# Kernel tuning notes

Hardware: AMD Instinct MI355X
Metric: run time of the kernel (lower is better)

The kernel has to match this reference:

```python
import jax, jax.numpy as jnp
import numpy as np

H, DH = 8, 64           # heads, dim_head
SCALE = DH ** -0.5


def setup_inputs() -> dict:
    key = jax.random.key(0)
    ks = jax.random.split(key, 8)
    b, f, n, dim = 16, 8, 256, 512
    inner = H * DH
    w = lambda k, s: jax.random.normal(k, s, jnp.float32) * 0.02
    return {
        "x": jax.random.normal(ks[0], (b, f * n, dim), jnp.float32),
        "external": jax.random.normal(ks[1], (b, 1, dim), jnp.float32),
        "Wq": w(ks[2], (dim, inner)), "bq": jnp.zeros((inner,), jnp.float32),
        "Wk": w(ks[3], (dim, inner)), "bk": jnp.zeros((inner,), jnp.float32),
        "Wv": w(ks[4], (dim, inner)), "bv": jnp.zeros((inner,), jnp.float32),
        "Wo": w(ks[5], (inner, dim)), "bo": jnp.zeros((dim,), jnp.float32),
        "f": f,
    }


def reference(x, external, Wq, bq, Wk, bk, Wv, bv, Wo, bo, f):
    b, N, dim = x.shape          # N = f * n
    n = N // f
    xa = jnp.concatenate([external, x], axis=1)          # (b, N+1, dim)

    def proj(W, bias):
        t = xa @ W + bias                                # (b, N+1, H*DH)
        # 'b n (h d) -> (b h) n d'
        return t.reshape(b, N + 1, H, DH).transpose(0, 2, 1, 3).reshape(b * H, N + 1, DH)

    q = proj(Wq, bq) * SCALE
    k = proj(Wk, bk)
    v = proj(Wv, bv)

    def split_local(t):
        ext = jnp.repeat(t[:, :1], f, axis=0)            # (b*H*f, 1, DH)  'b n d -> (b r) n d'
        loc = t[:, 1:].reshape(b * H * f, n, DH)         # 'b (f n) d -> (b f) n d'
        return jnp.concatenate([ext, loc], axis=1)       # (b*H*f, n+1, DH)

    q_, k_, v_ = split_local(q), split_local(k), split_local(v)

    att = jax.nn.softmax(jnp.einsum('bid,bjd->bij', q_, k_), axis=-1)
    out = jnp.einsum('bij,bjd->bid', att, v_)            # (b*H*f, n+1, DH)

    # external token output: '(b h r) d -> b r (h d)' then take r == 1
    ext_out = out[:, 0].reshape(b, H, f, DH).transpose(0, 2, 1, 3).reshape(b, f, H * DH)
    ext_out = ext_out[:, 1:2]                            # (b, 1, H*DH)

    # local outputs: '(b f) n d -> b (f n) d' then '(b h) n d -> b n (h d)'
    main = out[:, 1:].reshape(b, H, N, DH).transpose(0, 2, 1, 3).reshape(b, N, H * DH)

    return main @ Wo + bo, ext_out @ Wo + bo
```

## Files before the change

### kernel.cpp

```cpp
#include <hip/hip_runtime.h>
#include <stdint.h>

#define ATT_SCALE 0.125f

typedef __attribute__((ext_vector_type(8))) short bhalf8;
typedef __attribute__((ext_vector_type(4))) float floatx4;
typedef __attribute__((ext_vector_type(16))) float floatx16;
typedef __attribute__((ext_vector_type(8))) unsigned short ush8;

__device__ __forceinline__ unsigned short f2bf(float f) {
  union { float f; unsigned int u; } v; v.f = f;
  unsigned int r = v.u + 0x7fffu + ((v.u >> 16) & 1u);
  return (unsigned short)(r >> 16);
}
__device__ __forceinline__ float bf2f(unsigned short u) {
  union { unsigned int u; float f; } v; v.u = ((unsigned int)u) << 16;
  return v.f;
}
__device__ __forceinline__ unsigned int pk2(float a, float b) {
  unsigned int r;
  asm("v_cvt_pk_bf16_f32 %0, %1, %2" : "=v"(r) : "v"(a), "v"(b));
  return r;
}
__device__ __forceinline__ void glds16(const void* g, void* l) {
  __builtin_amdgcn_global_load_lds(
      (__attribute__((address_space(1))) void*)g,
      (__attribute__((address_space(3))) void*)l, 16, 0, 0);
}

__global__ __launch_bounds__(256) void k_conv_w(
    const float* __restrict__ Wq, const float* __restrict__ Wk,
    const float* __restrict__ Wv, const float* __restrict__ Wo,
    const float* __restrict__ bq, const float* __restrict__ bk, const float* __restrict__ bv,
    unsigned short* __restrict__ Wqkvt, unsigned short* __restrict__ Wot,
    float* __restrict__ biasqkv) {
  int idx = blockIdx.x * 256 + threadIdx.x;
  {
    int nn = idx >> 9, k = idx & 511;
    const float* W = (nn < 512) ? Wq : ((nn < 1024) ? Wk : Wv);
    int n = nn & 511;
    Wqkvt[idx] = f2bf(W[k * 512 + n]);
  }
  if (idx < 512 * 512) {
    int n = idx >> 9, k = idx & 511;
    Wot[idx] = f2bf(Wo[k * 512 + n]);
  }
  if (idx < 1536) {
    biasqkv[idx] = (idx < 512) ? bq[idx] : ((idx < 1024) ? bk[idx - 512] : bv[idx - 1024]);
  }
}

__global__ __launch_bounds__(256) void k_ext_qkv(
    const float* __restrict__ ext,
    const float* __restrict__ Wq, const float* __restrict__ Wk, const float* __restrict__ Wv,
    const float* __restrict__ bq, const float* __restrict__ bk, const float* __restrict__ bv,
    float* __restrict__ EQKV) {
  int b = blockIdx.x / 6, c = blockIdx.x % 6;
  int nn = c * 256 + threadIdx.x;
  __shared__ float xs[512];
  xs[threadIdx.x] = ext[b * 512 + threadIdx.x];
  xs[256 + threadIdx.x] = ext[b * 512 + 256 + threadIdx.x];
  __syncthreads();
  const float* W; const float* bias; float scale = 1.f; int n;
  if (nn < 512)      { W = Wq; bias = bq; n = nn;        scale = ATT_SCALE; }
  else if (nn < 1024){ W = Wk; bias = bk; n = nn - 512; }
  else               { W = Wv; bias = bv; n = nn - 1024; }
  float acc = 0.f;
  #pragma unroll 8
  for (int k = 0; k < 512; ++k) acc += xs[k] * W[k * 512 + n];
  EQKV[b * 1536 + nn] = (acc + bias[n]) * scale;
}

__global__ __launch_bounds__(256, 2) void k_gemm_qkv(
    const float* __restrict__ X, const unsigned short* __restrict__ B,
    const float* __restrict__ bias, unsigned short* __restrict__ C) {
  __shared__ __align__(16) float Af[8192];
  __shared__ __align__(16) unsigned short Bs[8192];
  int tid = threadIdx.x, lane = tid & 63, wv = tid >> 6;
  int lo = lane & 15, hi = lane >> 4;
  int waveM = wv >> 1, waveN = wv & 1;

  int nwg = gridDim.x;
  int wg = (blockIdx.x & 7) * (nwg >> 3) + (blockIdx.x >> 3);
  int bm = wg / 12, bn = wg % 12;

  const float* Xb = X + (size_t)bm * 128 * 512;
  const unsigned short* Bb = B + (size_t)bn * 128 * 512;

  floatx4 acc[4][4];
  #pragma unroll
  for (int m = 0; m < 4; ++m)
    #pragma unroll
    for (int n = 0; n < 4; ++n) acc[m][n] = floatx4{0.f, 0.f, 0.f, 0.f};

  for (int kt = 0; kt < 8; ++kt) {
    __syncthreads();
    #pragma unroll
    for (int i = 0; i < 8; ++i) {
      int chunk = i * 256 + tid;
      int row = chunk >> 4, slot = chunk & 15;
      glds16(Xb + (size_t)row * 512 + kt * 64 + ((slot ^ (row & 15)) << 2),
             Af + (size_t)(i * 256 + wv * 64) * 4);
    }
    #pragma unroll
    for (int i = 0; i < 4; ++i) {
      int chunk = i * 256 + tid;
      int row = chunk >> 3, slot = chunk & 7;
      glds16(Bb + (size_t)row * 512 + kt * 64 + ((slot ^ (row & 7)) << 3),
             Bs + (size_t)(i * 256 + wv * 64) * 8);
    }
    __syncthreads();

    bhalf8 af[4][2], bf4[4][2];
    #pragma unroll
    for (int m = 0; m < 4; ++m) {
      int row = waveM * 64 + m * 16 + lo;
      #pragma unroll
      for (int ks = 0; ks < 2; ++ks) {
        int j0 = (ks * 4 + hi) * 2;
        float4 fa = *(const float4*)(Af + (size_t)row * 64 + ((j0 ^ (row & 15)) << 2));
        float4 fb = *(const float4*)(Af + (size_t)row * 64 + (((j0 + 1) ^ (row & 15)) << 2));
        unsigned int* w = (unsigned int*)&af[m][ks];
        w[0] = pk2(fa.x, fa.y); w[1] = pk2(fa.z, fa.w);
        w[2] = pk2(fb.x, fb.y); w[3] = pk2(fb.z, fb.w);
      }
    }
    #pragma unroll
    for (int n = 0; n < 4; ++n) {
      int row = waveN * 64 + n * 16 + lo;
      #pragma unroll
      for (int ks = 0; ks < 2; ++ks)
        bf4[n][ks] = *(const bhalf8*)(Bs + (size_t)row * 64 + (((ks * 4 + hi) ^ (row & 7)) << 3));
    }
    #pragma unroll
    for (int m = 0; m < 4; ++m)
      #pragma unroll
      for (int n = 0; n < 4; ++n) {
        acc[m][n] = __builtin_amdgcn_mfma_f32_16x16x32_bf16(af[m][0], bf4[n][0], acc[m][n], 0, 0, 0);
        acc[m][n] = __builtin_amdgcn_mfma_f32_16x16x32_bf16(af[m][1], bf4[n][1], acc[m][n], 0, 0, 0);
      }
  }

  #pragma unroll
  for (int m = 0; m < 4; ++m) {
    int row0 = bm * 128 + waveM * 64 + m * 16 + hi * 4;
    #pragma unroll
    for (int n = 0; n < 4; ++n) {
      int col = bn * 128 + waveN * 64 + n * 16 + lo;
      float bb = bias[col];
      #pragma unroll
      for (int r = 0; r < 4; ++r) {
        float v = acc[m][n][r] + bb;
        if (col < 512) v *= ATT_SCALE;
        C[(size_t)(row0 + r) * 1536 + col] = f2bf(v);
      }
    }
  }
}

__global__ __launch_bounds__(256, 2) void k_gemm_out(
    const unsigned short* __restrict__ A, const unsigned short* __restrict__ B,
    const float* __restrict__ bias, float* __restrict__ C) {
  __shared__ __align__(16) unsigned short S[16384];
  int tid = threadIdx.x, lane = tid & 63, wv = tid >> 6;
  int lo = lane & 15, hi = lane >> 4;
  int waveM = wv >> 1, waveN = wv & 1;

  int nwg = gridDim.x;
  int wg = (blockIdx.x & 7) * (nwg >> 3) + (blockIdx.x >> 3);
  int bm = wg / 4, bn = wg % 4;

  const unsigned short* Ab = A + (size_t)bm * 128 * 512;
  const unsigned short* Bb = B + (size_t)bn * 128 * 512;
  unsigned short* lA = S;
  unsigned short* lB = S + 8192;

  floatx4 acc[4][4];
  #pragma unroll
  for (int m = 0; m < 4; ++m)
    #pragma unroll
    for (int n = 0; n < 4; ++n) acc[m][n] = floatx4{0.f, 0.f, 0.f, 0.f};

  for (int kt = 0; kt < 8; ++kt) {
    __syncthreads();
    #pragma unroll
    for (int i = 0; i < 4; ++i) {
      int chunk = i * 256 + tid;
      int row = chunk >> 3, slot = chunk & 7;
      glds16(Ab + (size_t)row * 512 + kt * 64 + ((slot ^ (row & 7)) << 3),
             lA + (size_t)(i * 256 + wv * 64) * 8);
    }
    #pragma unroll
    for (int i = 0; i < 4; ++i) {
      int chunk = i * 256 + tid;
      int row = chunk >> 3, slot = chunk & 7;
      glds16(Bb + (size_t)row * 512 + kt * 64 + ((slot ^ (row & 7)) << 3),
             lB + (size_t)(i * 256 + wv * 64) * 8);
    }
    __syncthreads();

    bhalf8 af[4][2], bf4[4][2];
    #pragma unroll
    for (int m = 0; m < 4; ++m) {
      int row = waveM * 64 + m * 16 + lo;
      #pragma unroll
      for (int ks = 0; ks < 2; ++ks)
        af[m][ks] = *(const bhalf8*)(lA + (size_t)row * 64 + (((ks * 4 + hi) ^ (row & 7)) << 3));
    }
    #pragma unroll
    for (int n = 0; n < 4; ++n) {
      int row = waveN * 64 + n * 16 + lo;
      #pragma unroll
      for (int ks = 0; ks < 2; ++ks)
        bf4[n][ks] = *(const bhalf8*)(lB + (size_t)row * 64 + (((ks * 4 + hi) ^ (row & 7)) << 3));
    }
    #pragma unroll
    for (int m = 0; m < 4; ++m)
      #pragma unroll
      for (int n = 0; n < 4; ++n) {
        acc[m][n] = __builtin_amdgcn_mfma_f32_16x16x32_bf16(af[m][0], bf4[n][0], acc[m][n], 0, 0, 0);
        acc[m][n] = __builtin_amdgcn_mfma_f32_16x16x32_bf16(af[m][1], bf4[n][1], acc[m][n], 0, 0, 0);
      }
  }

  #pragma unroll
  for (int m = 0; m < 4; ++m) {
    int row0 = bm * 128 + waveM * 64 + m * 16 + hi * 4;
    #pragma unroll
    for (int n = 0; n < 4; ++n) {
      int col = bn * 128 + waveN * 64 + n * 16 + lo;
      float bb = bias[col];
      #pragma unroll
      for (int r = 0; r < 4; ++r)
        C[(size_t)(row0 + r) * 512 + col] = acc[m][n][r] + bb;
    }
  }
}

#define VTC 296
__global__ __launch_bounds__(512, 4) void k_attn(
    const unsigned short* __restrict__ QKV,
    const float* __restrict__ EQKV,
    unsigned short* __restrict__ mainb) {
  __shared__ __align__(16) unsigned short Ks[256 * 64];
  __shared__ __align__(16) unsigned short Vt[64 * VTC];
  __shared__ float kx[64], vx[64];
  int g = blockIdx.x;
  int b = g >> 6, h = (g >> 3) & 7, j = g & 7;
  int tid = threadIdx.x, lane = tid & 63, wv = tid >> 6;
  int ql = lane & 31, hb = lane >> 5;
  const size_t rowbase = (size_t)b * 2048 + (size_t)j * 256;
  const unsigned short* Kg = QKV + rowbase * 1536 + 512 + h * 64;
  const unsigned short* Vg = QKV + rowbase * 1536 + 1024 + h * 64;

  int qbase = wv * 32;
  const unsigned short* qp = QKV + (rowbase + qbase + ql) * 1536 + h * 64 + hb * 8;
  bhalf8 qf[4];
  #pragma unroll
  for (int c = 0; c < 4; ++c) qf[c] = *(const bhalf8*)(qp + c * 16);

  {
    int keybase = wv * 32;
    #pragma unroll
    for (int i = 0; i < 4; ++i) {
      int key = keybase + i * 8 + (lane >> 3);
      int slot = lane & 7;
      const unsigned short* src =
          Kg + (size_t)key * 1536 + (((slot * 16) ^ ((key & 7) << 4)) >> 1);
      glds16(src, &Ks[(size_t)(keybase + i * 8) * 64]);
    }
  }
  for (int c = tid; c < 2048; c += 512) {
    int key = c & 255, d0 = (c >> 8) * 8;
    ush8 vv = *(const ush8*)(Vg + (size_t)key * 1536 + d0);
    #pragma unroll
    for (int u = 0; u < 8; ++u) Vt[(d0 + u) * VTC + key] = vv[u];
  }
  if (tid < 64) {
    kx[tid] = EQKV[b * 1536 + 512 + h * 64 + tid];
    vx[tid] = EQKV[b * 1536 + 1024 + h * 64 + tid];
  }
  __syncthreads();

  float part = 0.f;
  #pragma unroll
  for (int c = 0; c < 4; ++c)
    #pragma unroll
    for (int u = 0; u < 8; ++u)
      part += bf2f((unsigned short)qf[c][u]) * kx[c * 16 + hb * 8 + u];
  float m = part + __shfl_xor(part, 32, 64);
  float lsum = 1.f;
  floatx16 o0, o1;
  #pragma unroll
  for (int i = 0; i < 8; ++i) {
    int d0 = ((2 * i) & 3) + 8 * (i >> 1) + 4 * hb;
    o0[2 * i] = vx[d0];       o0[2 * i + 1] = vx[d0 + 1];
    o1[2 * i] = vx[32 + d0];  o1[2 * i + 1] = vx[32 + d0 + 1];
  }

  #pragma unroll
  for (int t = 0; t < 8; ++t) {
    floatx16 s;
    #pragma unroll
    for (int i = 0; i < 16; ++i) s[i] = 0.f;
    int key = t * 32 + ql;
    __builtin_amdgcn_s_setprio(1);
    #pragma unroll
    for (int c = 0; c < 4; ++c) {
      bhalf8 kf = *(const bhalf8*)((const char*)Ks + key * 128 +
                                   ((c * 32 + hb * 16) ^ ((key & 7) << 4)));
      s = __builtin_amdgcn_mfma_f32_32x32x16_bf16(kf, qf[c], s, 0, 0, 0);
    }
    __builtin_amdgcn_s_setprio(0);
    float mt = s[0];
    #pragma unroll
    for (int r = 1; r < 16; ++r) mt = fmaxf(mt, s[r]);
    mt = fmaxf(mt, __shfl_xor(mt, 32, 64));
    if (!__all(mt - m <= 8.f)) {
      float mnew = fmaxf(m, mt);
      float corr = __expf(m - mnew);
      lsum *= corr;
      #pragma unroll
      for (int r = 0; r < 16; ++r) { o0[r] *= corr; o1[r] *= corr; }
      m = mnew;
    }
    float p[16]; float ts = 0.f;
    #pragma unroll
    for (int r = 0; r < 16; ++r) { p[r] = __expf(s[r] - m); ts += p[r]; }
    lsum += ts;
    unsigned int pk[8], qk[8];
    #pragma unroll
    for (int i = 0; i < 8; ++i) pk[i] = pk2(p[2 * i], p[2 * i + 1]);
    #pragma unroll
    for (int i = 0; i < 8; ++i) qk[i] = __shfl_xor(pk[i], 32, 64);
    bhalf8 f0, f1;
    unsigned int* f0u = (unsigned int*)&f0;
    unsigned int* f1u = (unsigned int*)&f1;
    if (hb == 0) {
      f0u[0] = pk[0]; f0u[1] = pk[1]; f0u[2] = qk[0]; f0u[3] = qk[1];
      f1u[0] = pk[4]; f1u[1] = pk[5]; f1u[2] = qk[4]; f1u[3] = qk[5];
    } else {
      f0u[0] = qk[2]; f0u[1] = qk[3]; f0u[2] = pk[2]; f0u[3] = pk[3];
      f1u[0] = qk[6]; f1u[1] = qk[7]; f1u[2] = pk[6]; f1u[3] = pk[7];
    }
    {
      const char* vb0 = (const char*)Vt + ((0 * 32 + ql) * VTC + t * 32 + hb * 8) * 2;
      bhalf8 v0 = *(const bhalf8*)vb0;
      bhalf8 v1 = *(const bhalf8*)(vb0 + 32);
      const char* vb1 = (const char*)Vt + ((1 * 32 + ql) * VTC + t * 32 + hb * 8) * 2;
      bhalf8 w0 = *(const bhalf8*)vb1;
      bhalf8 w1 = *(const bhalf8*)(vb1 + 32);
      __builtin_amdgcn_s_setprio(1);
      o0 = __builtin_amdgcn_mfma_f32_32x32x16_bf16(v0, f0, o0, 0, 0, 0);
      o0 = __builtin_amdgcn_mfma_f32_32x32x16_bf16(v1, f1, o0, 0, 0, 0);
      o1 = __builtin_amdgcn_mfma_f32_32x32x16_bf16(w0, f0, o1, 0, 0, 0);
      o1 = __builtin_amdgcn_mfma_f32_32x32x16_bf16(w1, f1, o1, 0, 0, 0);
      __builtin_amdgcn_s_setprio(0);
    }
  }

  lsum += __shfl_xor(lsum, 32, 64);
  float rinv = 1.f / lsum;
  __syncthreads();
  char* ob = (char*)(Ks + wv * 2048);
  #pragma unroll
  for (int dt = 0; dt < 2; ++dt) {
    #pragma unroll
    for (int i = 0; i < 8; ++i) {
      int d0 = dt * 32 + ((2 * i) & 3) + 8 * (i >> 1) + 4 * hb;
      float a = (dt ? o1[2 * i] : o0[2 * i]) * rinv;
      float c = (dt ? o1[2 * i + 1] : o0[2 * i + 1]) * rinv;
      *(unsigned int*)(ob + ql * 128 + ((d0 * 2) ^ ((ql & 7) << 4))) = pk2(a, c);
    }
  }
  #pragma unroll
  for (int i = 0; i < 4; ++i) {
    int chunk = i * 64 + lane;
    int q = chunk >> 3, slot = chunk & 7;
    bhalf8 vv = *(const bhalf8*)(ob + q * 128 + ((slot * 16) ^ ((q & 7) << 4)));
    *(bhalf8*)(mainb + (rowbase + qbase + q) * 512 + h * 64 + slot * 8) = vv;
  }
}

__global__ __launch_bounds__(256) void k_ext_attn(
    const unsigned short* __restrict__ QKV, const float* __restrict__ EQKV,
    float* __restrict__ extpre) {
  int b = blockIdx.x >> 3, h = blockIdx.x & 7;
  int tid = threadIdx.x, lane = tid & 63, wv = tid >> 6;
  __shared__ float qs[64];
  __shared__ float ps[257];
  __shared__ float red[8];
  __shared__ float acc4[4][64];
  if (tid < 64) qs[tid] = EQKV[b * 1536 + h * 64 + tid];
  __syncthreads();
  const size_t base = (size_t)b * 2048 + 256;
  float sc[2] = {-1e30f, -1e30f};
  #pragma unroll
  for (int it = 0; it < 2; ++it) {
    int key = tid + it * 256;
    if (key < 257) {
      float s = 0.f;
      if (key == 0) {
        const float* kr = EQKV + b * 1536 + 512 + h * 64;
        #pragma unroll 8
        for (int d = 0; d < 64; ++d) s += qs[d] * kr[d];
      } else {
        const unsigned short* kr = QKV + (base + key - 1) * 1536 + 512 + h * 64;
        #pragma unroll
        for (int c = 0; c < 8; ++c) {
          ush8 kv = *(const ush8*)(kr + c * 8);
          #pragma unroll
          for (int u = 0; u < 8; ++u) s += qs[c * 8 + u] * bf2f(kv[u]);
        }
      }
      sc[it] = s;
    }
  }
  float lmax = fmaxf(sc[0], sc[1]);
  for (int d = 1; d < 64; d <<= 1) lmax = fmaxf(lmax, __shfl_xor(lmax, d, 64));
  if (lane == 0) red[wv] = lmax;
  __syncthreads();
  float M = fmaxf(fmaxf(red[0], red[1]), fmaxf(red[2], red[3]));
  float lsum = 0.f;
  #pragma unroll
  for (int it = 0; it < 2; ++it) {
    int key = tid + it * 256;
    if (key < 257) { float p = __expf(sc[it] - M); ps[key] = p; lsum += p; }
  }
  for (int d = 1; d < 64; d <<= 1) lsum += __shfl_xor(lsum, d, 64);
  if (lane == 0) red[4 + wv] = lsum;
  __syncthreads();
  float S = red[4] + red[5] + red[6] + red[7];
  int d = tid & 63, part = tid >> 6;
  float acc = 0.f;
  for (int key = part; key < 257; key += 4) {
    float vv = (key == 0) ? EQKV[b * 1536 + 1024 + h * 64 + d]
                          : bf2f(QKV[(base + key - 1) * 1536 + 1024 + h * 64 + d]);
    acc += ps[key] * vv;
  }
  acc4[part][d] = acc;
  __syncthreads();
  if (tid < 64) {
    float r = (acc4[0][tid] + acc4[1][tid] + acc4[2][tid] + acc4[3][tid]) / S;
    extpre[b * 512 + h * 64 + tid] = r;
  }
}

__global__ __launch_bounds__(256) void k_ext_out(
    const float* __restrict__ extpre, const float* __restrict__ Wo,
    const float* __restrict__ bo, float* __restrict__ out) {
  int b = blockIdx.x, half = blockIdx.y;
  int n = half * 256 + threadIdx.x;
  __shared__ float xs[512];
  xs[threadIdx.x] = extpre[b * 512 + threadIdx.x];
  xs[256 + threadIdx.x] = extpre[b * 512 + 256 + threadIdx.x];
  __syncthreads();
  float acc = bo[n];
  #pragma unroll 8
  for (int k = 0; k < 512; ++k) acc += xs[k] * Wo[k * 512 + n];
  out[16777216 + b * 512 + n] = acc;
}

extern "C" void kernel_launch(void* const* d_in, const int* in_sizes, int n_in,
                              void* d_out, int out_size, void* d_ws, size_t ws_size,
                              hipStream_t stream) {
  (void)in_sizes; (void)n_in; (void)out_size; (void)ws_size;
  const float* x   = (const float*)d_in[0];
  const float* ext = (const float*)d_in[1];
  const float* Wq  = (const float*)d_in[2];
  const float* bq  = (const float*)d_in[3];
  const float* Wk  = (const float*)d_in[4];
  const float* bk  = (const float*)d_in[5];
  const float* Wv  = (const float*)d_in[6];
  const float* bv  = (const float*)d_in[7];
  const float* Wo  = (const float*)d_in[8];
  const float* bo  = (const float*)d_in[9];
  float* out = (float*)d_out;

  char* ws = (char*)d_ws;
  size_t off = 0;
  auto take = [&](size_t bytes) { char* p = ws + off; off += (bytes + 255) & ~(size_t)255; return p; };
  unsigned short* Wqkvt  = (unsigned short*)take((size_t)1536 * 512 * 2);
  unsigned short* Wot    = (unsigned short*)take((size_t)512 * 512 * 2);
  float*          biasqkv= (float*)take(1536 * 4);
  float*          EQKV   = (float*)take(16 * 1536 * 4);
  unsigned short* QKVb   = (unsigned short*)take((size_t)32768 * 1536 * 2);
  unsigned short* mainb  = (unsigned short*)take((size_t)32768 * 512 * 2);
  float*          extpre = (float*)take(16 * 512 * 4);

  k_conv_w<<<3072, 256, 0, stream>>>(Wq, Wk, Wv, Wo, bq, bk, bv, Wqkvt, Wot, biasqkv);
  k_ext_qkv<<<96, 256, 0, stream>>>(ext, Wq, Wk, Wv, bq, bk, bv, EQKV);
  k_gemm_qkv<<<3072, 256, 0, stream>>>(x, Wqkvt, biasqkv, QKVb);
  k_attn<<<1024, 512, 0, stream>>>(QKVb, EQKV, mainb);
  k_ext_attn<<<128, 256, 0, stream>>>(QKVb, EQKV, extpre);
  k_gemm_out<<<1024, 256, 0, stream>>>(mainb, Wot, bo, out);
  k_ext_out<<<dim3(16, 2), 256, 0, stream>>>(extpre, Wo, bo, out);
}
```

Baseline: 224.6 us.

## Pre-convert X to bf16 and merge small ext kernels into main launches

```diff
diff --git a/kernel.cpp b/kernel.cpp
--- a/kernel.cpp
+++ b/kernel.cpp
@@ -28,54 +28,57 @@
       (__attribute__((address_space(3))) void*)l, 16, 0, 0);
 }
 
-__global__ __launch_bounds__(256) void k_conv_w(
+__global__ __launch_bounds__(256) void k_prep(
+    const float* __restrict__ x, const float* __restrict__ ext,
     const float* __restrict__ Wq, const float* __restrict__ Wk,
     const float* __restrict__ Wv, const float* __restrict__ Wo,
     const float* __restrict__ bq, const float* __restrict__ bk, const float* __restrict__ bv,
-    unsigned short* __restrict__ Wqkvt, unsigned short* __restrict__ Wot,
-    float* __restrict__ biasqkv) {
-  int idx = blockIdx.x * 256 + threadIdx.x;
-  {
-    int nn = idx >> 9, k = idx & 511;
-    const float* W = (nn < 512) ? Wq : ((nn < 1024) ? Wk : Wv);
-    int n = nn & 511;
-    Wqkvt[idx] = f2bf(W[k * 512 + n]);
-  }
-  if (idx < 512 * 512) {
-    int n = idx >> 9, k = idx & 511;
-    Wot[idx] = f2bf(Wo[k * 512 + n]);
-  }
-  if (idx < 1536) {
-    biasqkv[idx] = (idx < 512) ? bq[idx] : ((idx < 1024) ? bk[idx - 512] : bv[idx - 1024]);
-  }
-}
-
-__global__ __launch_bounds__(256) void k_ext_qkv(
-    const float* __restrict__ ext,
-    const float* __restrict__ Wq, const float* __restrict__ Wk, const float* __restrict__ Wv,
-    const float* __restrict__ bq, const float* __restrict__ bk, const float* __restrict__ bv,
+    unsigned short* __restrict__ Xbf, unsigned short* __restrict__ Wqkvt,
+    unsigned short* __restrict__ Wot, float* __restrict__ biasqkv,
     float* __restrict__ EQKV) {
-  int b = blockIdx.x / 6, c = blockIdx.x % 6;
-  int nn = c * 256 + threadIdx.x;
   __shared__ float xs[512];
-  xs[threadIdx.x] = ext[b * 512 + threadIdx.x];
-  xs[256 + threadIdx.x] = ext[b * 512 + 256 + threadIdx.x];
-  __syncthreads();
-  const float* W; const float* bias; float scale = 1.f; int n;
-  if (nn < 512)      { W = Wq; bias = bq; n = nn;        scale = ATT_SCALE; }
-  else if (nn < 1024){ W = Wk; bias = bk; n = nn - 512; }
-  else               { W = Wv; bias = bv; n = nn - 1024; }
-  float acc = 0.f;
-  #pragma unroll 8
-  for (int k = 0; k < 512; ++k) acc += xs[k] * W[k * 512 + n];
-  EQKV[b * 1536 + nn] = (acc + bias[n]) * scale;
+  int bid = blockIdx.x, tid = threadIdx.x;
+  if (bid < 16384) {
+    int i = bid * 256 + tid;
+    float4 v = ((const float4*)x)[i];
+    ((uint2*)Xbf)[i] = make_uint2(pk2(v.x, v.y), pk2(v.z, v.w));
+  } else if (bid < 19456) {
+    int idx = (bid - 16384) * 256 + tid;
+    {
+      int nn = idx >> 9, k = idx & 511;
+      const float* W = (nn < 512) ? Wq : ((nn < 1024) ? Wk : Wv);
+      int n = nn & 511;
+      Wqkvt[idx] = f2bf(W[k * 512 + n]);
+    }
+    if (idx < 512 * 512) {
+      int n = idx >> 9, k = idx & 511;
+      Wot[idx] = f2bf(Wo[k * 512 + n]);
+    }
+    if (idx < 1536) {
+      biasqkv[idx] = (idx < 512) ? bq[idx] : ((idx < 1024) ? bk[idx - 512] : bv[idx - 1024]);
+    }
+  } else {
+    int bid2 = bid - 19456;
+    int b = bid2 / 6, c = bid2 % 6;
+    int nn = c * 256 + tid;
+    xs[tid] = ext[b * 512 + tid];
+    xs[256 + tid] = ext[b * 512 + 256 + tid];
+    __syncthreads();
+    const float* W; const float* bias; float scale = 1.f; int n;
+    if (nn < 512)      { W = Wq; bias = bq; n = nn;        scale = ATT_SCALE; }
+    else if (nn < 1024){ W = Wk; bias = bk; n = nn - 512; }
+    else               { W = Wv; bias = bv; n = nn - 1024; }
+    float acc = 0.f;
+    #pragma unroll 8
+    for (int k = 0; k < 512; ++k) acc += xs[k] * W[k * 512 + n];
+    EQKV[b * 1536 + nn] = (acc + bias[n]) * scale;
+  }
 }
 
 __global__ __launch_bounds__(256, 2) void k_gemm_qkv(
-    const float* __restrict__ X, const unsigned short* __restrict__ B,
+    const unsigned short* __restrict__ A, const unsigned short* __restrict__ B,
     const float* __restrict__ bias, unsigned short* __restrict__ C) {
-  __shared__ __align__(16) float Af[8192];
-  __shared__ __align__(16) unsigned short Bs[8192];
+  __shared__ __align__(16) unsigned short S[16384];
   int tid = threadIdx.x, lane = tid & 63, wv = tid >> 6;
   int lo = lane & 15, hi = lane >> 4;
   int waveM = wv >> 1, waveN = wv & 1;
@@ -84,8 +87,10 @@
   int wg = (blockIdx.x & 7) * (nwg >> 3) + (blockIdx.x >> 3);
   int bm = wg / 12, bn = wg % 12;
 
-  const float* Xb = X + (size_t)bm * 128 * 512;
+  const unsigned short* Ab = A + (size_t)bm * 128 * 512;
   const unsigned short* Bb = B + (size_t)bn * 128 * 512;
+  unsigned short* lA = S;
+  unsigned short* lB = S + 8192;
 
   floatx4 acc[4][4];
   #pragma unroll
@@ -96,18 +101,18 @@
   for (int kt = 0; kt < 8; ++kt) {
     __syncthreads();
     #pragma unroll
-    for (int i = 0; i < 8; ++i) {
+    for (int i = 0; i < 4; ++i) {
       int chunk = i * 256 + tid;
-      int row = chunk >> 4, slot = chunk & 15;
-      glds16(Xb + (size_t)row * 512 + kt * 64 + ((slot ^ (row & 15)) << 2),
-             Af + (size_t)(i * 256 + wv * 64) * 4);
+      int row = chunk >> 3, slot = chunk & 7;
+      glds16(Ab + (size_t)row * 512 + kt * 64 + ((slot ^ (row & 7)) << 3),
+             lA + (size_t)(i * 256 + wv * 64) * 8);
     }
     #pragma unroll
     for (int i = 0; i < 4; ++i) {
       int chunk = i * 256 + tid;
       int row = chunk >> 3, slot = chunk & 7;
       glds16(Bb + (size_t)row * 512 + kt * 64 + ((slot ^ (row & 7)) << 3),
-             Bs + (size_t)(i * 256 + wv * 64) * 8);
+             lB + (size_t)(i * 256 + wv * 64) * 8);
     }
     __syncthreads();
 
@@ -116,21 +121,15 @@
     for (int m = 0; m < 4; ++m) {
       int row = waveM * 64 + m * 16 + lo;
       #pragma unroll
-      for (int ks = 0; ks < 2; ++ks) {
-        int j0 = (ks * 4 + hi) * 2;
-        float4 fa = *(const float4*)(Af + (size_t)row * 64 + ((j0 ^ (row & 15)) << 2));
-        float4 fb = *(const float4*)(Af + (size_t)row * 64 + (((j0 + 1) ^ (row & 15)) << 2));
-        unsigned int* w = (unsigned int*)&af[m][ks];
-        w[0] = pk2(fa.x, fa.y); w[1] = pk2(fa.z, fa.w);
-        w[2] = pk2(fb.x, fb.y); w[3] = pk2(fb.z, fb.w);
-      }
+      for (int ks = 0; ks < 2; ++ks)
+        af[m][ks] = *(const bhalf8*)(lA + (size_t)row * 64 + (((ks * 4 + hi) ^ (row & 7)) << 3));
     }
     #pragma unroll
     for (int n = 0; n < 4; ++n) {
       int row = waveN * 64 + n * 16 + lo;
       #pragma unroll
       for (int ks = 0; ks < 2; ++ks)
-        bf4[n][ks] = *(const bhalf8*)(Bs + (size_t)row * 64 + (((ks * 4 + hi) ^ (row & 7)) << 3));
+        bf4[n][ks] = *(const bhalf8*)(lB + (size_t)row * 64 + (((ks * 4 + hi) ^ (row & 7)) << 3));
     }
     #pragma unroll
     for (int m = 0; m < 4; ++m)
@@ -158,96 +157,78 @@
   }
 }
 
-__global__ __launch_bounds__(256, 2) void k_gemm_out(
-    const unsigned short* __restrict__ A, const unsigned short* __restrict__ B,
-    const float* __restrict__ bias, float* __restrict__ C) {
-  __shared__ __align__(16) unsigned short S[16384];
-  int tid = threadIdx.x, lane = tid & 63, wv = tid >> 6;
-  int lo = lane & 15, hi = lane >> 4;
-  int waveM = wv >> 1, waveN = wv & 1;
-
-  int nwg = gridDim.x;
-  int wg = (blockIdx.x & 7) * (nwg >> 3) + (blockIdx.x >> 3);
-  int bm = wg / 4, bn = wg % 4;
-
-  const unsigned short* Ab = A + (size_t)bm * 128 * 512;
-  const unsigned short* Bb = B + (size_t)bn * 128 * 512;
-  unsigned short* lA = S;
-  unsigned short* lB = S + 8192;
-
-  floatx4 acc[4][4];
-  #pragma unroll
-  for (int m = 0; m < 4; ++m)
-    #pragma unroll
-    for (int n = 0; n < 4; ++n) acc[m][n] = floatx4{0.f, 0.f, 0.f, 0.f};
-
-  for (int kt = 0; kt < 8; ++kt) {
-    __syncthreads();
-    #pragma unroll
-    for (int i = 0; i < 4; ++i) {
-      int chunk = i * 256 + tid;
-      int row = chunk >> 3, slot = chunk & 7;
-      glds16(Ab + (size_t)row * 512 + kt * 64 + ((slot ^ (row & 7)) << 3),
-             lA + (size_t)(i * 256 + wv * 64) * 8);
-    }
-    #pragma unroll
-    for (int i = 0; i < 4; ++i) {
-      int chunk = i * 256 + tid;
-      int row = chunk >> 3, slot = chunk & 7;
-      glds16(Bb + (size_t)row * 512 + kt * 64 + ((slot ^ (row & 7)) << 3),
-             lB + (size_t)(i * 256 + wv * 64) * 8);
-    }
-    __syncthreads();
-
-    bhalf8 af[4][2], bf4[4][2];
-    #pragma unroll
-    for (int m = 0; m < 4; ++m) {
-      int row = waveM * 64 + m * 16 + lo;
-      #pragma unroll
-      for (int ks = 0; ks < 2; ++ks)
-        af[m][ks] = *(const bhalf8*)(lA + (size_t)row * 64 + (((ks * 4 + hi) ^ (row & 7)) << 3));
-    }
-    #pragma unroll
-    for (int n = 0; n < 4; ++n) {
-      int row = waveN * 64 + n * 16 + lo;
-      #pragma unroll
-      for (int ks = 0; ks < 2; ++ks)
-        bf4[n][ks] = *(const bhalf8*)(lB + (size_t)row * 64 + (((ks * 4 + hi) ^ (row & 7)) << 3));
-    }
-    #pragma unroll
-    for (int m = 0; m < 4; ++m)
-      #pragma unroll
-      for (int n = 0; n < 4; ++n) {
-        acc[m][n] = __builtin_amdgcn_mfma_f32_16x16x32_bf16(af[m][0], bf4[n][0], acc[m][n], 0, 0, 0);
-        acc[m][n] = __builtin_amdgcn_mfma_f32_16x16x32_bf16(af[m][1], bf4[n][1], acc[m][n], 0, 0, 0);
-      }
-  }
-
-  #pragma unroll
-  for (int m = 0; m < 4; ++m) {
-    int row0 = bm * 128 + waveM * 64 + m * 16 + hi * 4;
-    #pragma unroll
-    for (int n = 0; n < 4; ++n) {
-      int col = bn * 128 + waveN * 64 + n * 16 + lo;
-      float bb = bias[col];
-      #pragma unroll
-      for (int r = 0; r < 4; ++r)
-        C[(size_t)(row0 + r) * 512 + col] = acc[m][n][r] + bb;
-    }
-  }
-}
-
 #define VTC 296
-__global__ __launch_bounds__(512, 4) void k_attn(
+__global__ __launch_bounds__(512, 4) void k_attn_all(
     const unsigned short* __restrict__ QKV,
     const float* __restrict__ EQKV,
-    unsigned short* __restrict__ mainb) {
+    unsigned short* __restrict__ mainb,
+    float* __restrict__ extpre) {
   __shared__ __align__(16) unsigned short Ks[256 * 64];
   __shared__ __align__(16) unsigned short Vt[64 * VTC];
   __shared__ float kx[64], vx[64];
+  int tid = threadIdx.x, lane = tid & 63, wv = tid >> 6;
+
+  if (blockIdx.x >= 1024) {
+    int eg = blockIdx.x - 1024;
+    int b = eg >> 3, h = eg & 7;
+    float* qs   = (float*)Ks;
+    float* ps   = qs + 64;
+    float* redm = ps + 257;
+    float* reds = redm + 8;
+    float (*acc8)[64] = (float (*)[64])(reds + 8);
+    if (tid < 64) qs[tid] = EQKV[b * 1536 + h * 64 + tid];
+    __syncthreads();
+    const size_t base = (size_t)b * 2048 + 256;
+    float s = -1e30f;
+    if (tid < 257) {
+      s = 0.f;
+      if (tid == 0) {
+        const float* kr = EQKV + b * 1536 + 512 + h * 64;
+        #pragma unroll 8
+        for (int d = 0; d < 64; ++d) s += qs[d] * kr[d];
+      } else {
+        const unsigned short* kr = QKV + (base + tid - 1) * 1536 + 512 + h * 64;
+        #pragma unroll
+        for (int c = 0; c < 8; ++c) {
+          ush8 kv = *(const ush8*)(kr + c * 8);
+          #pragma unroll
+          for (int u = 0; u < 8; ++u) s += qs[c * 8 + u] * bf2f(kv[u]);
+        }
+      }
+    }
+    float lmax = s;
+    for (int d = 1; d < 64; d <<= 1) lmax = fmaxf(lmax, __shfl_xor(lmax, d, 64));
+    if (lane == 0) redm[wv] = lmax;
+    __syncthreads();
+    float M = redm[0];
+    #pragma unroll
+    for (int w = 1; w < 8; ++w) M = fmaxf(M, redm[w]);
+    float p = 0.f;
+    if (tid < 257) { p = __expf(s - M); ps[tid] = p; }
+    float lsum = p;
+    for (int d = 1; d < 64; d <<= 1) lsum += __shfl_xor(lsum, d, 64);
+    if (lane == 0) reds[wv] = lsum;
+    __syncthreads();
+    float Ssum = reds[0] + reds[1] + reds[2] + reds[3] + reds[4] + reds[5] + reds[6] + reds[7];
+    int d = tid & 63, part = tid >> 6;
+    float acc = 0.f;
+    for (int key = part; key < 257; key += 8) {
+      float vv = (key == 0) ? EQKV[b * 1536 + 1024 + h * 64 + d]
+                            : bf2f(QKV[(base + key - 1) * 1536 + 1024 + h * 64 + d]);
+      acc += ps[key] * vv;
+    }
+    acc8[part][d] = acc;
+    __syncthreads();
+    if (tid < 64) {
+      float r = (acc8[0][tid] + acc8[1][tid] + acc8[2][tid] + acc8[3][tid] +
+                 acc8[4][tid] + acc8[5][tid] + acc8[6][tid] + acc8[7][tid]) / Ssum;
+      extpre[b * 512 + h * 64 + tid] = r;
+    }
+    return;
+  }
+
   int g = blockIdx.x;
   int b = g >> 6, h = (g >> 3) & 7, j = g & 7;
-  int tid = threadIdx.x, lane = tid & 63, wv = tid >> 6;
   int ql = lane & 31, hb = lane >> 5;
   const size_t rowbase = (size_t)b * 2048 + (size_t)j * 256;
   const unsigned short* Kg = QKV + rowbase * 1536 + 512 + h * 64;
@@ -382,83 +363,99 @@
   }
 }
 
-__global__ __launch_bounds__(256) void k_ext_attn(
-    const unsigned short* __restrict__ QKV, const float* __restrict__ EQKV,
-    float* __restrict__ extpre) {
-  int b = blockIdx.x >> 3, h = blockIdx.x & 7;
+__global__ __launch_bounds__(256, 2) void k_gemm_out(
+    const unsigned short* __restrict__ A, const unsigned short* __restrict__ B,
+    const float* __restrict__ bias, float* __restrict__ C,
+    const float* __restrict__ extpre, const float* __restrict__ Wo) {
+  __shared__ __align__(16) unsigned short S[16384];
   int tid = threadIdx.x, lane = tid & 63, wv = tid >> 6;
-  __shared__ float qs[64];
-  __shared__ float ps[257];
-  __shared__ float red[8];
-  __shared__ float acc4[4][64];
-  if (tid < 64) qs[tid] = EQKV[b * 1536 + h * 64 + tid];
-  __syncthreads();
-  const size_t base = (size_t)b * 2048 + 256;
-  float sc[2] = {-1e30f, -1e30f};
-  #pragma unroll
-  for (int it = 0; it < 2; ++it) {
-    int key = tid + it * 256;
-    if (key < 257) {
-      float s = 0.f;
-      if (key == 0) {
-        const float* kr = EQKV + b * 1536 + 512 + h * 64;
-        #pragma unroll 8
-        for (int d = 0; d < 64; ++d) s += qs[d] * kr[d];
-      } else {
-        const unsigned short* kr = QKV + (base + key - 1) * 1536 + 512 + h * 64;
-        #pragma unroll
-        for (int c = 0; c < 8; ++c) {
-          ush8 kv = *(const ush8*)(kr + c * 8);
-          #pragma unroll
-          for (int u = 0; u < 8; ++u) s += qs[c * 8 + u] * bf2f(kv[u]);
-        }
+  int nwg = gridDim.x;
+  int wg = (blockIdx.x & 7) * (nwg >> 3) + (blockIdx.x >> 3);
+
+  if (wg >= 1024) {
+    int idx = wg - 1024;
+    int b = idx >> 1, half = idx & 1;
+    int n = half * 256 + tid;
+    float* xs = (float*)S;
+    xs[tid] = extpre[b * 512 + tid];
+    xs[256 + tid] = extpre[b * 512 + 256 + tid];
+    __syncthreads();
+    float acc = bias[n];
+    #pragma unroll 8
+    for (int k = 0; k < 512; ++k) acc += xs[k] * Wo[k * 512 + n];
+    C[16777216 + b * 512 + n] = acc;
+    return;
+  }
+
+  int lo = lane & 15, hi = lane >> 4;
+  int waveM = wv >> 1, waveN = wv & 1;
+  int bm = wg / 4, bn = wg % 4;
+
+  const unsigned short* Ab = A + (size_t)bm * 128 * 512;
+  const unsigned short* Bb = B + (size_t)bn * 128 * 512;
+  unsigned short* lA = S;
+  unsigned short* lB = S + 8192;
+
+  floatx4 acc[4][4];
+  #pragma unroll
+  for (int m = 0; m < 4; ++m)
+    #pragma unroll
+    for (int n = 0; n < 4; ++n) acc[m][n] = floatx4{0.f, 0.f, 0.f, 0.f};
+
+  for (int kt = 0; kt < 8; ++kt) {
+    __syncthreads();
+    #pragma unroll
+    for (int i = 0; i < 4; ++i) {
+      int chunk = i * 256 + tid;
+      int row = chunk >> 3, slot = chunk & 7;
+      glds16(Ab + (size_t)row * 512 + kt * 64 + ((slot ^ (row & 7)) << 3),
+             lA + (size_t)(i * 256 + wv * 64) * 8);
+    }
+    #pragma unroll
+    for (int i = 0; i < 4; ++i) {
+      int chunk = i * 256 + tid;
+      int row = chunk >> 3, slot = chunk & 7;
+      glds16(Bb + (size_t)row * 512 + kt * 64 + ((slot ^ (row & 7)) << 3),
+             lB + (size_t)(i * 256 + wv * 64) * 8);
+    }
+    __syncthreads();
+
+    bhalf8 af[4][2], bf4[4][2];
+    #pragma unroll
+    for (int m = 0; m < 4; ++m) {
+      int row = waveM * 64 + m * 16 + lo;
+      #pragma unroll
+      for (int ks = 0; ks < 2; ++ks)
+        af[m][ks] = *(const bhalf8*)(lA + (size_t)row * 64 + (((ks * 4 + hi) ^ (row & 7)) << 3));
+    }
+    #pragma unroll
+    for (int n = 0; n < 4; ++n) {
+      int row = waveN * 64 + n * 16 + lo;
+      #pragma unroll
+      for (int ks = 0; ks < 2; ++ks)
+        bf4[n][ks] = *(const bhalf8*)(lB + (size_t)row * 64 + (((ks * 4 + hi) ^ (row & 7)) << 3));
+    }
+    #pragma unroll
+    for (int m = 0; m < 4; ++m)
+      #pragma unroll
+      for (int n = 0; n < 4; ++n) {
+        acc[m][n] = __builtin_amdgcn_mfma_f32_16x16x32_bf16(af[m][0], bf4[n][0], acc[m][n], 0, 0, 0);
+        acc[m][n] = __builtin_amdgcn_mfma_f32_16x16x32_bf16(af[m][1], bf4[n][1], acc[m][n], 0, 0, 0);
       }
-      sc[it] = s;
-    }
-  }
-  float lmax = fmaxf(sc[0], sc[1]);
-  for (int d = 1; d < 64; d <<= 1) lmax = fmaxf(lmax, __shfl_xor(lmax, d, 64));
-  if (lane == 0) red[wv] = lmax;
-  __syncthreads();
-  float M = fmaxf(fmaxf(red[0], red[1]), fmaxf(red[2], red[3]));
-  float lsum = 0.f;
-  #pragma unroll
-  for (int it = 0; it < 2; ++it) {
-    int key = tid + it * 256;
-    if (key < 257) { float p = __expf(sc[it] - M); ps[key] = p; lsum += p; }
-  }
-  for (int d = 1; d < 64; d <<= 1) lsum += __shfl_xor(lsum, d, 64);
-  if (lane == 0) red[4 + wv] = lsum;
-  __syncthreads();
-  float S = red[4] + red[5] + red[6] + red[7];
-  int d = tid & 63, part = tid >> 6;
-  float acc = 0.f;
-  for (int key = part; key < 257; key += 4) {
-    float vv = (key == 0) ? EQKV[b * 1536 + 1024 + h * 64 + d]
-                          : bf2f(QKV[(base + key - 1) * 1536 + 1024 + h * 64 + d]);
-    acc += ps[key] * vv;
-  }
-  acc4[part][d] = acc;
-  __syncthreads();
-  if (tid < 64) {
-    float r = (acc4[0][tid] + acc4[1][tid] + acc4[2][tid] + acc4[3][tid]) / S;
-    extpre[b * 512 + h * 64 + tid] = r;
-  }
-}
-
-__global__ __launch_bounds__(256) void k_ext_out(
-    const float* __restrict__ extpre, const float* __restrict__ Wo,
-    const float* __restrict__ bo, float* __restrict__ out) {
-  int b = blockIdx.x, half = blockIdx.y;
-  int n = half * 256 + threadIdx.x;
-  __shared__ float xs[512];
-  xs[threadIdx.x] = extpre[b * 512 + threadIdx.x];
-  xs[256 + threadIdx.x] = extpre[b * 512 + 256 + threadIdx.x];
-  __syncthreads();
-  float acc = bo[n];
-  #pragma unroll 8
-  for (int k = 0; k < 512; ++k) acc += xs[k] * Wo[k * 512 + n];
-  out[16777216 + b * 512 + n] = acc;
+  }
+
+  #pragma unroll
+  for (int m = 0; m < 4; ++m) {
+    int row0 = bm * 128 + waveM * 64 + m * 16 + hi * 4;
+    #pragma unroll
+    for (int n = 0; n < 4; ++n) {
+      int col = bn * 128 + waveN * 64 + n * 16 + lo;
+      float bb = bias[col];
+      #pragma unroll
+      for (int r = 0; r < 4; ++r)
+        C[(size_t)(row0 + r) * 512 + col] = acc[m][n][r] + bb;
+    }
+  }
 }
 
 extern "C" void kernel_launch(void* const* d_in, const int* in_sizes, int n_in,
@@ -480,6 +477,7 @@
   char* ws = (char*)d_ws;
   size_t off = 0;
   auto take = [&](size_t bytes) { char* p = ws + off; off += (bytes + 255) & ~(size_t)255; return p; };
+  unsigned short* Xbf    = (unsigned short*)take((size_t)32768 * 512 * 2);
   unsigned short* Wqkvt  = (unsigned short*)take((size_t)1536 * 512 * 2);
   unsigned short* Wot    = (unsigned short*)take((size_t)512 * 512 * 2);
   float*          biasqkv= (float*)take(1536 * 4);
@@ -488,11 +486,9 @@
   unsigned short* mainb  = (unsigned short*)take((size_t)32768 * 512 * 2);
   float*          extpre = (float*)take(16 * 512 * 4);
 
-  k_conv_w<<<3072, 256, 0, stream>>>(Wq, Wk, Wv, Wo, bq, bk, bv, Wqkvt, Wot, biasqkv);
-  k_ext_qkv<<<96, 256, 0, stream>>>(ext, Wq, Wk, Wv, bq, bk, bv, EQKV);
-  k_gemm_qkv<<<3072, 256, 0, stream>>>(x, Wqkvt, biasqkv, QKVb);
-  k_attn<<<1024, 512, 0, stream>>>(QKVb, EQKV, mainb);
-  k_ext_attn<<<128, 256, 0, stream>>>(QKVb, EQKV, extpre);
-  k_gemm_out<<<1024, 256, 0, stream>>>(mainb, Wot, bo, out);
-  k_ext_out<<<dim3(16, 2), 256, 0, stream>>>(extpre, Wo, bo, out);
-}
+  k_prep<<<19552, 256, 0, stream>>>(x, ext, Wq, Wk, Wv, Wo, bq, bk, bv,
+                                    Xbf, Wqkvt, Wot, biasqkv, EQKV);
+  k_gemm_qkv<<<3072, 256, 0, stream>>>(Xbf, Wqkvt, biasqkv, QKVb);
+  k_attn_all<<<1152, 512, 0, stream>>>(QKVb, EQKV, mainb, extpre);
+  k_gemm_out<<<1056, 256, 0, stream>>>(mainb, Wot, bo, out, extpre, Wo);
+}
```

Measured after the change: 180.3 us (median of 2 runs). -19.7%, faster.
